# Performance work log

Measured on AMD Instinct MI355X. Metric: run time of the kernel, lower is better.

Reference implementation:

```python
import jax, jax.numpy as jnp
import numpy as np

N = 100000   # num nodes
E = 1200000  # num edges
D = 64       # hidden_channel == middle_channel
ALPHA = 0.5
LN_EPS = 1e-5


def setup_inputs() -> dict:
    key = jax.random.key(0)
    ks = jax.random.split(key, 8)
    z = jax.random.normal(ks[0], (N, D), jnp.float32)
    x = jax.random.normal(ks[1], (N, D), jnp.float32)
    edge_index = jax.random.randint(ks[2], (2, E), 0, N)
    norm_factor = jax.random.uniform(ks[3], (N, 1), jnp.float32)  # >0 a.s.
    s = 0.1
    W = jax.random.normal(ks[4], (D, D), jnp.float32) * s    # nn.Linear(hidden, hidden, bias=False).weight
    U_w = jax.random.normal(ks[5], (D, D), jnp.float32) * s  # nn.Linear(hidden, middle).weight
    U_b = jax.random.normal(ks[6], (D,), jnp.float32) * s    # nn.Linear(hidden, middle).bias
    ln_gamma = jnp.ones((D,), jnp.float32)
    ln_beta = jnp.zeros((D,), jnp.float32)
    return dict(z=z, x=x, edge_index=edge_index, norm_factor=norm_factor,
                W=W, U_w=U_w, U_b=U_b, ln_gamma=ln_gamma, ln_beta=ln_beta)


def reference(z, x, edge_index, norm_factor, W, U_w, U_b, ln_gamma, ln_beta):
    row, col = edge_index[0], edge_index[1]
    # rescale=True: degree = 1/norm_factor with inf -> 0 (safe division)
    safe_nf = jnp.where(norm_factor > 0, norm_factor, 1.0)
    degree = jnp.where(norm_factor > 0, 1.0 / safe_nf, 0.0)  # [N,1]
    # double_linear=True: W(z) + degree * U(x), then graph-norm scale
    WzUx = z @ W.T + degree * (x @ U_w.T + U_b)  # [N,D]
    WzUx = norm_factor * WzUx
    # edge diff (gather), act + LayerNorm (batch=None path)
    e = WzUx[row] - WzUx[col]                    # [E,D]
    e = jax.nn.relu(e)
    mu = jnp.mean(e, axis=-1, keepdims=True)
    var = jnp.var(e, axis=-1, keepdims=True)
    e = (e - mu) * jax.lax.rsqrt(var + LN_EPS) * ln_gamma + ln_beta
    # double scatter_add aggregation
    new_z = jax.ops.segment_sum(e * norm_factor[row], row, num_segments=N)
    new_z = new_z - jax.ops.segment_sum(e * norm_factor[col], col, num_segments=N)
    # -F.linear(new_z, W.t()) == -(new_z @ W)
    new_z = -(new_z @ W)
    # dropout p=0.0 -> identity
    return ALPHA * new_z + (1.0 - ALPHA) * z
```

## Files before the change

### kernel.cpp

```cpp
#include <hip/hip_runtime.h>

#define D 64
#define LN_EPS 1e-5f
#define ALPHA 0.5f

#define GB 64
#define GSH 6
#define NSUB 8
#define CAPS 320
#define CAP 2048

__device__ __forceinline__ unsigned xcc_id() {
    unsigned v;
    asm volatile("s_getreg_b32 %0, hwreg(HW_REG_XCC_ID)" : "=s"(v));
    return v & (NSUB - 1);
}

__global__ __launch_bounds__(256) void wzux_kernel(
    const float* __restrict__ z, const float* __restrict__ x,
    const float* __restrict__ nf, const float* __restrict__ W,
    const float* __restrict__ Uw, const float* __restrict__ Ub,
    float* __restrict__ wzux, int N)
{
    const int lane = threadIdx.x & 63;
    const int wid  = threadIdx.x >> 6;

    float4 wreg[16], ureg[16];
    {
        const float4* wr = (const float4*)(W  + (size_t)lane * D);
        const float4* ur = (const float4*)(Uw + (size_t)lane * D);
#pragma unroll
        for (int i = 0; i < 16; ++i) { wreg[i] = wr[i]; ureg[i] = ur[i]; }
    }
    const float ub = Ub[lane];

    for (int n = blockIdx.x * 4 + wid; n < N; n += gridDim.x * 4) {
        const int un = __builtin_amdgcn_readfirstlane(n);
        const float4* zr = (const float4*)(z + (size_t)un * D);
        const float4* xr = (const float4*)(x + (size_t)un * D);
        float accw = 0.f, accu = 0.f;
#pragma unroll
        for (int c = 0; c < 16; ++c) {
            float4 zc = zr[c];
            float4 xc = xr[c];
            accw = fmaf(zc.x, wreg[c].x, accw);
            accw = fmaf(zc.y, wreg[c].y, accw);
            accw = fmaf(zc.z, wreg[c].z, accw);
            accw = fmaf(zc.w, wreg[c].w, accw);
            accu = fmaf(xc.x, ureg[c].x, accu);
            accu = fmaf(xc.y, ureg[c].y, accu);
            accu = fmaf(xc.z, ureg[c].z, accu);
            accu = fmaf(xc.w, ureg[c].w, accu);
        }
        float nfv = nf[un];
        float deg = (nfv > 0.f) ? (1.f / nfv) : 0.f;
        wzux[(size_t)un * D + lane] = nfv * (accw + deg * (accu + ub));
    }
}

__global__ __launch_bounds__(256) void bucket_scatter_kernel(
    const int* __restrict__ row, const int* __restrict__ col,
    int* __restrict__ cursor, int* __restrict__ data, int E)
{
    int i = blockIdx.x * blockDim.x + threadIdx.x;
    if (i >= E) return;
    const int sub = xcc_id();
    int r = row[i], c = col[i];

    int br = r >> GSH;
    int sr = atomicAdd(&cursor[br * NSUB + sub], 1);
    if (sr < CAPS)
        data[(br * NSUB + sub) * CAPS + sr] = (c << 7) | ((r & (GB - 1)) << 1);

    int bc = c >> GSH;
    int sc = atomicAdd(&cursor[bc * NSUB + sub], 1);
    if (sc < CAPS)
        data[(bc * NSUB + sub) * CAPS + sc] = (r << 7) | ((c & (GB - 1)) << 1) | 1;
}

__global__ __launch_bounds__(256) void bucket_sort_agg_kernel(
    const float4* __restrict__ wzux4,
    const int* __restrict__ cursor, const int* __restrict__ data,
    const float* __restrict__ nf,
    const float4* __restrict__ gamma4, const float4* __restrict__ beta4,
    float4* __restrict__ out4, int N)
{
    __shared__ int sorted[CAP];
    __shared__ int offs[GB + 1];
    __shared__ int curs[GB];

    const int b    = blockIdx.x;
    const int base = b << GSH;
    const int cntN = min(GB, N - base);
    const int t    = threadIdx.x;

    const int* bcur  = &cursor[b * NSUB];
    const int* bdata = &data[(size_t)b * NSUB * CAPS];

    if (t < GB + 1) offs[t] = 0;
    __syncthreads();

    for (int sub = 0; sub < NSUB; ++sub) {
        const int cs = min(bcur[sub], CAPS);
        for (int i = t; i < cs; i += 256) {
            int local = (bdata[sub * CAPS + i] >> 1) & (GB - 1);
            atomicAdd(&offs[local + 1], 1);
        }
    }
    __syncthreads();

    if (t < GB) {
        int v = offs[t + 1];
#pragma unroll
        for (int off = 1; off < GB; off <<= 1) {
            int u = __shfl_up(v, off);
            if (t >= off) v += u;
        }
        offs[t + 1] = v;
    }
    __syncthreads();
    if (t < GB) curs[t] = offs[t];
    __syncthreads();

    for (int sub = 0; sub < NSUB; ++sub) {
        const int cs = min(bcur[sub], CAPS);
        for (int i = t; i < cs; i += 256) {
            int ent = bdata[sub * CAPS + i];
            int local = (ent >> 1) & (GB - 1);
            int p = atomicAdd(&curs[local], 1);
            if (p < CAP) sorted[p] = ent;
        }
    }
    __syncthreads();

    const int lane = t & 63;
    const int wid  = t >> 6;
    const int g = lane >> 4;
    const int l = lane & 15;
    const float4 gm = gamma4[l];
    const float4 bt = beta4[l];

    for (int local = wid; local < cntN; local += 4) {
        const int s = offs[local];
        const int e = min(offs[local + 1], CAP);
        const int n = base + local;
        const float4 self = wzux4[n * 16 + l];
        float4 acc = make_float4(0.f, 0.f, 0.f, 0.f);

#define PROC2(ENT, OROW)                                                     \
        {                                                                    \
            int ent = (ENT);                                                 \
            float sgn = (ent & 1) ? -1.f : 1.f;                              \
            float4 o = (OROW);                                               \
            float r0 = fmaxf(sgn * (self.x - o.x), 0.f);                     \
            float r1 = fmaxf(sgn * (self.y - o.y), 0.f);                     \
            float r2 = fmaxf(sgn * (self.z - o.z), 0.f);                     \
            float r3 = fmaxf(sgn * (self.w - o.w), 0.f);                     \
            float ss = r0 + r1 + r2 + r3;                                    \
            float sq = r0 * r0 + r1 * r1 + r2 * r2 + r3 * r3;                \
            _Pragma("unroll")                                                \
            for (int off = 1; off < 16; off <<= 1) {                         \
                ss += __shfl_xor(ss, off);                                   \
                sq += __shfl_xor(sq, off);                                   \
            }                                                                \
            float mu   = ss * (1.f / 64.f);                                  \
            float var  = sq * (1.f / 64.f) - mu * mu;                        \
            float rstd = rsqrtf(var + LN_EPS);                               \
            acc.x += sgn * ((r0 - mu) * rstd * gm.x + bt.x);                 \
            acc.y += sgn * ((r1 - mu) * rstd * gm.y + bt.y);                 \
            acc.z += sgn * ((r2 - mu) * rstd * gm.z + bt.z);                 \
            acc.w += sgn * ((r3 - mu) * rstd * gm.w + bt.w);                 \
        }

        int i = s + g;
        for (; i + 4 < e; i += 8) {
            int ea = sorted[i];
            int eb = sorted[i + 4];
            float4 oa = wzux4[(ea >> 7) * 16 + l];
            float4 ob = wzux4[(eb >> 7) * 16 + l];
            PROC2(ea, oa);
            PROC2(eb, ob);
        }
        if (i < e) {
            int ea = sorted[i];
            float4 oa = wzux4[(ea >> 7) * 16 + l];
            PROC2(ea, oa);
        }
#undef PROC2

#pragma unroll
        for (int m = 16; m < 64; m <<= 1) {
            acc.x += __shfl_xor(acc.x, m);
            acc.y += __shfl_xor(acc.y, m);
            acc.z += __shfl_xor(acc.z, m);
            acc.w += __shfl_xor(acc.w, m);
        }

        if (g == 0) {
            float nfv = nf[n];
            out4[n * 16 + l] = make_float4(acc.x * nfv, acc.y * nfv,
                                           acc.z * nfv, acc.w * nfv);
        }
    }
}

__global__ __launch_bounds__(256) void out_kernel(
    const float* accv, const float* __restrict__ z,
    const float* __restrict__ W, float* out, int N)
{
    const int lane = threadIdx.x & 63;
    const int wid  = threadIdx.x >> 6;

    float wcol[D];
#pragma unroll
    for (int k = 0; k < D; ++k) wcol[k] = W[k * D + lane];

    for (int n = blockIdx.x * 4 + wid; n < N; n += gridDim.x * 4) {
        const int un = __builtin_amdgcn_readfirstlane(n);
        const float4* ar = (const float4*)(accv + (size_t)un * D);
        float acc = 0.f;
#pragma unroll
        for (int c = 0; c < 16; ++c) {
            float4 a = ar[c];
            acc = fmaf(a.x, wcol[c * 4 + 0], acc);
            acc = fmaf(a.y, wcol[c * 4 + 1], acc);
            acc = fmaf(a.z, wcol[c * 4 + 2], acc);
            acc = fmaf(a.w, wcol[c * 4 + 3], acc);
        }
        out[(size_t)un * D + lane] =
            (1.0f - ALPHA) * z[(size_t)un * D + lane] - ALPHA * acc;
    }
}

extern "C" void kernel_launch(void* const* d_in, const int* in_sizes, int n_in,
                              void* d_out, int out_size, void* d_ws, size_t ws_size,
                              hipStream_t stream) {
    const float* z     = (const float*)d_in[0];
    const float* x     = (const float*)d_in[1];
    const int*   ei    = (const int*)d_in[2];
    const float* nf    = (const float*)d_in[3];
    const float* W     = (const float*)d_in[4];
    const float* Uw    = (const float*)d_in[5];
    const float* Ub    = (const float*)d_in[6];
    const float* gamma = (const float*)d_in[7];
    const float* beta  = (const float*)d_in[8];

    const int N = in_sizes[0] / D;
    const int E = in_sizes[2] / 2;
    const int NBK = (N + GB - 1) >> GSH;

    float* out = (float*)d_out;

    char* ws = (char*)d_ws;
    size_t off = 0;
    auto alloc = [&](size_t bytes) {
        char* p = ws + off;
        off += (bytes + 255) & ~(size_t)255;
        return p;
    };
    float* wzux   = (float*)alloc((size_t)N * D * sizeof(float));
    int*   cursor = (int*)  alloc((size_t)NBK * NSUB * sizeof(int));
    int*   bdata  = (int*)  alloc((size_t)NBK * NSUB * CAPS * sizeof(int));

    hipMemsetAsync(cursor, 0, (size_t)NBK * NSUB * sizeof(int), stream);

    wzux_kernel<<<1024, 256, 0, stream>>>(z, x, nf, W, Uw, Ub, wzux, N);

    int eb = (E + 255) / 256;
    bucket_scatter_kernel<<<eb, 256, 0, stream>>>(ei, ei + E, cursor, bdata, E);

    bucket_sort_agg_kernel<<<NBK, 256, 0, stream>>>(
        (const float4*)wzux, cursor, bdata, nf,
        (const float4*)gamma, (const float4*)beta,
        (float4*)out, N);

    out_kernel<<<1024, 256, 0, stream>>>(out, z, W, out, N);
}
```

Baseline: 383.5 us.

## Replace per-edge global atomics with tiled two-pass radix scatter into coarser buckets

The edge bucketing now processes 2048-edge tiles per block. It counts per-bucket occupancy in shared memory, reserves global space with one atomic per bucket, then writes records, so global atomic traffic drops sharply. Buckets grow to 256 nodes with an overflow list in place of silent drops. The aggregation kernel has four blocks read each coarse bucket and keep only their 64-node quarter, which means each block scans roughly four times as much bucket data. The wzux kernel splits the W and U products across lanes, and both matvec kernels use four independent FMA accumulators to shorten dependency chains.

```diff
diff --git a/kernel.cpp b/kernel.cpp
--- a/kernel.cpp
+++ b/kernel.cpp
@@ -4,11 +4,14 @@
 #define LN_EPS 1e-5f
 #define ALPHA 0.5f
 
-#define GB 64
-#define GSH 6
+#define GSH 8
+#define GBN 256
 #define NSUB 8
-#define CAPS 320
-#define CAP 2048
+#define TILE 2048
+#define CAPS 1280
+#define CAPQ 1792
+#define OVF_CAP 131072
+#define MAXBUCK 400
 
 __device__ __forceinline__ unsigned xcc_id() {
     unsigned v;
@@ -24,111 +27,166 @@
 {
     const int lane = threadIdx.x & 63;
     const int wid  = threadIdx.x >> 6;
-
-    float4 wreg[16], ureg[16];
+    const int par  = blockIdx.x & 1;
+    const int half = lane >> 5;
+    const int d    = par * 32 + (lane & 31);
+
+    const float* M = half ? Uw : W;
+    float4 wreg[16];
     {
-        const float4* wr = (const float4*)(W  + (size_t)lane * D);
-        const float4* ur = (const float4*)(Uw + (size_t)lane * D);
-#pragma unroll
-        for (int i = 0; i < 16; ++i) { wreg[i] = wr[i]; ureg[i] = ur[i]; }
-    }
-    const float ub = Ub[lane];
-
-    for (int n = blockIdx.x * 4 + wid; n < N; n += gridDim.x * 4) {
+        const float4* wr = (const float4*)(M + (size_t)d * D);
+#pragma unroll
+        for (int i = 0; i < 16; ++i) wreg[i] = wr[i];
+    }
+    const float ub = Ub[d];
+    const float* base_src = half ? x : z;
+
+    const int start = (blockIdx.x >> 1) * 4 + wid;
+    const int step  = (gridDim.x >> 1) * 4;
+
+    for (int n = start; n < N; n += step) {
         const int un = __builtin_amdgcn_readfirstlane(n);
-        const float4* zr = (const float4*)(z + (size_t)un * D);
-        const float4* xr = (const float4*)(x + (size_t)un * D);
-        float accw = 0.f, accu = 0.f;
+        const float4* src = (const float4*)(base_src + (size_t)un * D);
+        float a0 = 0.f, a1 = 0.f, a2 = 0.f, a3 = 0.f;
 #pragma unroll
         for (int c = 0; c < 16; ++c) {
-            float4 zc = zr[c];
-            float4 xc = xr[c];
-            accw = fmaf(zc.x, wreg[c].x, accw);
-            accw = fmaf(zc.y, wreg[c].y, accw);
-            accw = fmaf(zc.z, wreg[c].z, accw);
-            accw = fmaf(zc.w, wreg[c].w, accw);
-            accu = fmaf(xc.x, ureg[c].x, accu);
-            accu = fmaf(xc.y, ureg[c].y, accu);
-            accu = fmaf(xc.z, ureg[c].z, accu);
-            accu = fmaf(xc.w, ureg[c].w, accu);
-        }
-        float nfv = nf[un];
-        float deg = (nfv > 0.f) ? (1.f / nfv) : 0.f;
-        wzux[(size_t)un * D + lane] = nfv * (accw + deg * (accu + ub));
-    }
-}
-
-__global__ __launch_bounds__(256) void bucket_scatter_kernel(
+            float4 v = src[c];
+            a0 = fmaf(v.x, wreg[c].x, a0);
+            a1 = fmaf(v.y, wreg[c].y, a1);
+            a2 = fmaf(v.z, wreg[c].z, a2);
+            a3 = fmaf(v.w, wreg[c].w, a3);
+        }
+        float acc = (a0 + a1) + (a2 + a3);
+        float other = __shfl_xor(acc, 32);
+        if (half == 0) {
+            float nfv = nf[un];
+            float deg = (nfv > 0.f) ? (1.f / nfv) : 0.f;
+            wzux[(size_t)un * D + d] = nfv * (acc + deg * (other + ub));
+        }
+    }
+}
+
+__global__ __launch_bounds__(256) void radix_scatter_kernel(
     const int* __restrict__ row, const int* __restrict__ col,
-    int* __restrict__ cursor, int* __restrict__ data, int E)
+    int* __restrict__ gcur, int* __restrict__ data,
+    int* __restrict__ ovf_cnt, int2* __restrict__ ovf,
+    int E, int nbuck)
 {
-    int i = blockIdx.x * blockDim.x + threadIdx.x;
-    if (i >= E) return;
-    const int sub = xcc_id();
-    int r = row[i], c = col[i];
-
-    int br = r >> GSH;
-    int sr = atomicAdd(&cursor[br * NSUB + sub], 1);
-    if (sr < CAPS)
-        data[(br * NSUB + sub) * CAPS + sr] = (c << 7) | ((r & (GB - 1)) << 1);
-
-    int bc = c >> GSH;
-    int sc = atomicAdd(&cursor[bc * NSUB + sub], 1);
-    if (sc < CAPS)
-        data[(bc * NSUB + sub) * CAPS + sc] = (r << 7) | ((c & (GB - 1)) << 1) | 1;
+    __shared__ int cnt[MAXBUCK];
+    __shared__ int gbase[MAXBUCK];
+    const int t  = threadIdx.x;
+    const int e0 = blockIdx.x * TILE;
+    const int e1 = min(e0 + TILE, E);
+    const unsigned sub = xcc_id();
+
+    for (int i = t; i < nbuck; i += 256) cnt[i] = 0;
+    __syncthreads();
+
+    for (int e = e0 + t; e < e1; e += 256) {
+        atomicAdd(&cnt[row[e] >> GSH], 1);
+        atomicAdd(&cnt[col[e] >> GSH], 1);
+    }
+    __syncthreads();
+
+    for (int b = t; b < nbuck; b += 256) {
+        int c = cnt[b];
+        gbase[b] = (c > 0) ? atomicAdd(&gcur[b * NSUB + sub], c) : 0;
+    }
+    __syncthreads();
+
+    for (int e = e0 + t; e < e1; e += 256) {
+        int r = row[e], c = col[e];
+        {
+            int b = r >> GSH;
+            int s = atomicSub(&cnt[b], 1) - 1;
+            int pos = gbase[b] + s;
+            int rec = (c << 9) | ((r & (GBN - 1)) << 1);
+            if (pos < CAPS) data[(b * NSUB + (int)sub) * CAPS + pos] = rec;
+            else { int o = atomicAdd(ovf_cnt, 1);
+                   if (o < OVF_CAP) ovf[o] = make_int2(b, rec); }
+        }
+        {
+            int b = c >> GSH;
+            int s = atomicSub(&cnt[b], 1) - 1;
+            int pos = gbase[b] + s;
+            int rec = (r << 9) | ((c & (GBN - 1)) << 1) | 1;
+            if (pos < CAPS) data[(b * NSUB + (int)sub) * CAPS + pos] = rec;
+            else { int o = atomicAdd(ovf_cnt, 1);
+                   if (o < OVF_CAP) ovf[o] = make_int2(b, rec); }
+        }
+    }
 }
 
 __global__ __launch_bounds__(256) void bucket_sort_agg_kernel(
     const float4* __restrict__ wzux4,
-    const int* __restrict__ cursor, const int* __restrict__ data,
+    const int* __restrict__ gcur, const int* __restrict__ data,
+    const int* __restrict__ ovf_cnt, const int2* __restrict__ ovf,
     const float* __restrict__ nf,
     const float4* __restrict__ gamma4, const float4* __restrict__ beta4,
     float4* __restrict__ out4, int N)
 {
-    __shared__ int sorted[CAP];
-    __shared__ int offs[GB + 1];
-    __shared__ int curs[GB];
-
-    const int b    = blockIdx.x;
-    const int base = b << GSH;
-    const int cntN = min(GB, N - base);
-    const int t    = threadIdx.x;
-
-    const int* bcur  = &cursor[b * NSUB];
-    const int* bdata = &data[(size_t)b * NSUB * CAPS];
-
-    if (t < GB + 1) offs[t] = 0;
-    __syncthreads();
+    __shared__ int sorted[CAPQ];
+    __shared__ int offs[65];
+    __shared__ int curs[64];
+
+    const int blk    = blockIdx.x;
+    const int base   = blk << 6;
+    const int cntN   = min(64, N - base);
+    const int bucket = blk >> 2;
+    const int q      = blk & 3;
+    const int t      = threadIdx.x;
+
+    if (t < 65) offs[t] = 0;
+    __syncthreads();
+
+    const int ocnt = min(*ovf_cnt, OVF_CAP);
 
     for (int sub = 0; sub < NSUB; ++sub) {
-        const int cs = min(bcur[sub], CAPS);
+        const int cs = min(gcur[bucket * NSUB + sub], CAPS);
+        const int* p = &data[(bucket * NSUB + sub) * CAPS];
         for (int i = t; i < cs; i += 256) {
-            int local = (bdata[sub * CAPS + i] >> 1) & (GB - 1);
-            atomicAdd(&offs[local + 1], 1);
-        }
-    }
-    __syncthreads();
-
-    if (t < GB) {
+            int l8 = (p[i] >> 1) & (GBN - 1);
+            if ((l8 >> 6) == q) atomicAdd(&offs[(l8 & 63) + 1], 1);
+        }
+    }
+    for (int i = t; i < ocnt; i += 256) {
+        int2 v = ovf[i];
+        int l8 = (v.y >> 1) & (GBN - 1);
+        if (v.x == bucket && (l8 >> 6) == q) atomicAdd(&offs[(l8 & 63) + 1], 1);
+    }
+    __syncthreads();
+
+    if (t < 64) {
         int v = offs[t + 1];
 #pragma unroll
-        for (int off = 1; off < GB; off <<= 1) {
+        for (int off = 1; off < 64; off <<= 1) {
             int u = __shfl_up(v, off);
             if (t >= off) v += u;
         }
         offs[t + 1] = v;
     }
     __syncthreads();
-    if (t < GB) curs[t] = offs[t];
+    if (t < 64) curs[t] = offs[t];
     __syncthreads();
 
     for (int sub = 0; sub < NSUB; ++sub) {
-        const int cs = min(bcur[sub], CAPS);
+        const int cs = min(gcur[bucket * NSUB + sub], CAPS);
+        const int* p = &data[(bucket * NSUB + sub) * CAPS];
         for (int i = t; i < cs; i += 256) {
-            int ent = bdata[sub * CAPS + i];
-            int local = (ent >> 1) & (GB - 1);
-            int p = atomicAdd(&curs[local], 1);
-            if (p < CAP) sorted[p] = ent;
+            int rec = p[i];
+            int l8 = (rec >> 1) & (GBN - 1);
+            if ((l8 >> 6) == q) {
+                int pos = atomicAdd(&curs[l8 & 63], 1);
+                if (pos < CAPQ) sorted[pos] = rec;
+            }
+        }
+    }
+    for (int i = t; i < ocnt; i += 256) {
+        int2 v = ovf[i];
+        int l8 = (v.y >> 1) & (GBN - 1);
+        if (v.x == bucket && (l8 >> 6) == q) {
+            int pos = atomicAdd(&curs[l8 & 63], 1);
+            if (pos < CAPQ) sorted[pos] = v.y;
         }
     }
     __syncthreads();
@@ -141,8 +199,8 @@
     const float4 bt = beta4[l];
 
     for (int local = wid; local < cntN; local += 4) {
-        const int s = offs[local];
-        const int e = min(offs[local + 1], CAP);
+        const int s = min(offs[local], CAPQ);
+        const int e = min(offs[local + 1], CAPQ);
         const int n = base + local;
         const float4 self = wzux4[n * 16 + l];
         float4 acc = make_float4(0.f, 0.f, 0.f, 0.f);
@@ -176,14 +234,14 @@
         for (; i + 4 < e; i += 8) {
             int ea = sorted[i];
             int eb = sorted[i + 4];
-            float4 oa = wzux4[(ea >> 7) * 16 + l];
-            float4 ob = wzux4[(eb >> 7) * 16 + l];
+            float4 oa = wzux4[(ea >> 9) * 16 + l];
+            float4 ob = wzux4[(eb >> 9) * 16 + l];
             PROC2(ea, oa);
             PROC2(eb, ob);
         }
         if (i < e) {
             int ea = sorted[i];
-            float4 oa = wzux4[(ea >> 7) * 16 + l];
+            float4 oa = wzux4[(ea >> 9) * 16 + l];
             PROC2(ea, oa);
         }
 #undef PROC2
@@ -218,15 +276,16 @@
     for (int n = blockIdx.x * 4 + wid; n < N; n += gridDim.x * 4) {
         const int un = __builtin_amdgcn_readfirstlane(n);
         const float4* ar = (const float4*)(accv + (size_t)un * D);
-        float acc = 0.f;
+        float a0 = 0.f, a1 = 0.f, a2 = 0.f, a3 = 0.f;
 #pragma unroll
         for (int c = 0; c < 16; ++c) {
             float4 a = ar[c];
-            acc = fmaf(a.x, wcol[c * 4 + 0], acc);
-            acc = fmaf(a.y, wcol[c * 4 + 1], acc);
-            acc = fmaf(a.z, wcol[c * 4 + 2], acc);
-            acc = fmaf(a.w, wcol[c * 4 + 3], acc);
-        }
+            a0 = fmaf(a.x, wcol[c * 4 + 0], a0);
+            a1 = fmaf(a.y, wcol[c * 4 + 1], a1);
+            a2 = fmaf(a.z, wcol[c * 4 + 2], a2);
+            a3 = fmaf(a.w, wcol[c * 4 + 3], a3);
+        }
+        float acc = (a0 + a1) + (a2 + a3);
         out[(size_t)un * D + lane] =
             (1.0f - ALPHA) * z[(size_t)un * D + lane] - ALPHA * acc;
     }
@@ -247,7 +306,7 @@
 
     const int N = in_sizes[0] / D;
     const int E = in_sizes[2] / 2;
-    const int NBK = (N + GB - 1) >> GSH;
+    const int nbuck = (N + GBN - 1) >> GSH;
 
     float* out = (float*)d_out;
 
@@ -258,21 +317,26 @@
         off += (bytes + 255) & ~(size_t)255;
         return p;
     };
-    float* wzux   = (float*)alloc((size_t)N * D * sizeof(float));
-    int*   cursor = (int*)  alloc((size_t)NBK * NSUB * sizeof(int));
-    int*   bdata  = (int*)  alloc((size_t)NBK * NSUB * CAPS * sizeof(int));
-
-    hipMemsetAsync(cursor, 0, (size_t)NBK * NSUB * sizeof(int), stream);
-
-    wzux_kernel<<<1024, 256, 0, stream>>>(z, x, nf, W, Uw, Ub, wzux, N);
-
-    int eb = (E + 255) / 256;
-    bucket_scatter_kernel<<<eb, 256, 0, stream>>>(ei, ei + E, cursor, bdata, E);
-
-    bucket_sort_agg_kernel<<<NBK, 256, 0, stream>>>(
-        (const float4*)wzux, cursor, bdata, nf,
+    float* wzux    = (float*)alloc((size_t)N * D * sizeof(float));
+    int*   gcur    = (int*)  alloc((size_t)nbuck * NSUB * sizeof(int));
+    int*   ovf_cnt = (int*)  alloc(sizeof(int));
+    int*   data    = (int*)  alloc((size_t)nbuck * NSUB * CAPS * sizeof(int));
+    int2*  ovf     = (int2*) alloc((size_t)OVF_CAP * sizeof(int2));
+
+    hipMemsetAsync(gcur, 0, (size_t)nbuck * NSUB * sizeof(int), stream);
+    hipMemsetAsync(ovf_cnt, 0, sizeof(int), stream);
+
+    wzux_kernel<<<2048, 256, 0, stream>>>(z, x, nf, W, Uw, Ub, wzux, N);
+
+    int sb = (E + TILE - 1) / TILE;
+    radix_scatter_kernel<<<sb, 256, 0, stream>>>(ei, ei + E, gcur, data,
+                                                 ovf_cnt, ovf, E, nbuck);
+
+    int ab = (N + 63) / 64;
+    bucket_sort_agg_kernel<<<ab, 256, 0, stream>>>(
+        (const float4*)wzux, gcur, data, ovf_cnt, ovf, nf,
         (const float4*)gamma, (const float4*)beta,
         (float4*)out, N);
 
-    out_kernel<<<1024, 256, 0, stream>>>(out, z, W, out, N);
-}
+    out_kernel<<<2048, 256, 0, stream>>>(out, z, W, out, N);
+}
```

New measurement: 341.4 us. 11.0% less time.
